# Performance work log

Hardware: AMD Instinct MI355X
Metric: run time of the kernel (lower is better)

## Reference

```python
import jax, jax.numpy as jnp
import numpy as np

IN_SIZE, R = 80, 5
D = 256  # hidden size used throughout
OUT = IN_SIZE * R  # 400


def gru_cell(x, h, Wih, Whh, bih, bhh):
    # torch.nn.GRUCell semantics
    gi = x @ Wih.T + bih
    gh = h @ Whh.T + bhh
    ir, iz, in_ = jnp.split(gi, 3, axis=-1)
    hr, hz, hn = jnp.split(gh, 3, axis=-1)
    r = jax.nn.sigmoid(ir + hr)
    z = jax.nn.sigmoid(iz + hz)
    n = jnp.tanh(in_ + r * hn)
    return (1.0 - z) * n + z * h


def setup_inputs() -> dict:
    key = jax.random.key(0)
    ks = jax.random.split(key, 32)
    s = 0.05
    inp = {
        'encoder_outputs': jax.random.normal(ks[0], (128, 512, D), jnp.float32),
        'inputs': jax.random.normal(ks[1], (128, 1000, IN_SIZE), jnp.float32),
        # Prenet: Linear(400,256), Linear(256,128)
        'W1': jax.random.normal(ks[2], (256, OUT)) * s, 'b1': jnp.zeros((256,)),
        'W2': jax.random.normal(ks[3], (128, 256)) * s, 'b2': jnp.zeros((128,)),
        # attn GRUCell(384 -> 256)
        'Wih_a': jax.random.normal(ks[4], (3 * D, 128 + D)) * s,
        'Whh_a': jax.random.normal(ks[5], (3 * D, D)) * s,
        'bih_a': jnp.zeros((3 * D,)), 'bhh_a': jnp.zeros((3 * D,)),
        # Bahdanau attention: query_layer (no bias) and v: Linear(256,1,no bias)
        'Wq': jax.random.normal(ks[6], (D, D)) * s,
        'v': jax.random.normal(ks[7], (D,)) * s,
        # memory_layer Linear(256,256,no bias)
        'Wm': jax.random.normal(ks[8], (D, D)) * s,
        # pre_rnn_dec_proj Linear(512,256)
        'Wp': jax.random.normal(ks[9], (D, 2 * D)) * s, 'bp': jnp.zeros((D,)),
        # two decoder GRUCells(256 -> 256)
        'Wih_d1': jax.random.normal(ks[10], (3 * D, D)) * s,
        'Whh_d1': jax.random.normal(ks[11], (3 * D, D)) * s,
        'bih_d1': jnp.zeros((3 * D,)), 'bhh_d1': jnp.zeros((3 * D,)),
        'Wih_d2': jax.random.normal(ks[12], (3 * D, D)) * s,
        'Whh_d2': jax.random.normal(ks[13], (3 * D, D)) * s,
        'bih_d2': jnp.zeros((3 * D,)), 'bhh_d2': jnp.zeros((3 * D,)),
        # mel projection Linear(256, 400)
        'Wmel': jax.random.normal(ks[14], (OUT, D)) * s, 'bmel': jnp.zeros((OUT,)),
    }
    return inp


def reference(encoder_outputs, inputs, W1, b1, W2, b2,
              Wih_a, Whh_a, bih_a, bhh_a, Wq, v, Wm, Wp, bp,
              Wih_d1, Whh_d1, bih_d1, bhh_d1,
              Wih_d2, Whh_d2, bih_d2, bhh_d2, Wmel, bmel):
    B = encoder_outputs.shape[0]
    processed_mem = encoder_outputs @ Wm.T               # (B, T_enc, D)
    # teacher forcing: (B, T_mel, in_size) -> (T_dec, B, in_size*r)
    x = inputs.reshape(B, inputs.shape[1] // R, -1).transpose(1, 0, 2)
    # decoder input at step t is frame t-1 (zeros at t=0)
    x_shift = jnp.concatenate([jnp.zeros_like(x[:1]), x[:-1]], axis=0)

    def step(carry, x_t):
        attn_h, h1, h2, ctx = carry
        # prenet (dropout disabled: eval-mode reference)
        pre = jax.nn.relu(x_t @ W1.T + b1)
        pre = jax.nn.relu(pre @ W2.T + b2)                # (B, 128)
        cell_in = jnp.concatenate([pre, ctx], axis=-1)    # (B, 384)
        attn_h = gru_cell(cell_in, attn_h, Wih_a, Whh_a, bih_a, bhh_a)
        q = attn_h @ Wq.T                                 # (B, D)
        logits = jnp.tanh(q[:, None, :] + processed_mem) @ v  # (B, T_enc)
        align = jax.nn.softmax(logits, axis=-1)
        ctx = jnp.einsum('bt,btd->bd', align, encoder_outputs)
        dec_in = jnp.concatenate([attn_h, ctx], axis=-1) @ Wp.T + bp
        h1 = gru_cell(dec_in, h1, Wih_d1, Whh_d1, bih_d1, bhh_d1)
        dec_in = h1 + dec_in
        h2 = gru_cell(dec_in, h2, Wih_d2, Whh_d2, bih_d2, bhh_d2)
        dec_in = h2 + dec_in
        out = dec_in @ Wmel.T + bmel                      # (B, 400)
        return (attn_h, h1, h2, ctx), (out, align)

    z = jnp.zeros((B, D), encoder_outputs.dtype)
    init = (z, z, z, z)
    _, (outs, aligns) = jax.lax.scan(step, init, x_shift)
    outputs = outs.transpose(1, 0, 2)       # (B, T_dec, 400)
    alignments = aligns.transpose(1, 0, 2)  # (B, T_dec, T_enc)
    return outputs, alignments
```

## Files before the change

kernel.cpp:

```cpp
#include <hip/hip_runtime.h>

typedef _Float16 h2f __attribute__((ext_vector_type(2)));

#define LOG2E 1.44269504088896f

__device__ __forceinline__ float fexp2(float x){ return __builtin_amdgcn_exp2f(x); }
__device__ __forceinline__ float frcp (float x){ return __builtin_amdgcn_rcpf(x); }
__device__ __forceinline__ float sigm (float x){ return frcp(1.f + fexp2(-LOG2E*x)); }
__device__ __forceinline__ float tanhf2(float x){
  x = fminf(15.f, fmaxf(-15.f, x));
  float e = fexp2(2.f*LOG2E*x);
  return (e-1.f)*frcp(e+1.f);
}
__device__ __forceinline__ unsigned pkh2(float a, float b){
  h2f h; h.x = (_Float16)a; h.y = (_Float16)b;
  return __builtin_bit_cast(unsigned, h);
}

#if __has_builtin(__builtin_amdgcn_fdot2)
__device__ __forceinline__ float dot2(unsigned a, unsigned b, float c){
  return __builtin_amdgcn_fdot2(__builtin_bit_cast(h2f,a), __builtin_bit_cast(h2f,b), c, false);
}
#else
__device__ __forceinline__ float dot2(unsigned a, unsigned b, float c){
  h2f ha=__builtin_bit_cast(h2f,a), hb=__builtin_bit_cast(h2f,b);
  return c + (float)ha.x*(float)hb.x + (float)ha.y*(float)hb.y;
}
#endif

__device__ __forceinline__ void dot8_2(uint4 w, uint4 x, float& a0, float& a1){
  a0 = dot2(w.x, x.x, a0); a1 = dot2(w.y, x.y, a1);
  a0 = dot2(w.z, x.z, a0); a1 = dot2(w.w, x.w, a1);
}

template<int N, int K8>
__device__ __forceinline__ float mv(const uint4* __restrict__ W, const uint4* __restrict__ xs, int n){
  float a0 = 0.f, a1 = 0.f;
  #pragma unroll 4
  for (int k8 = 0; k8 < K8; ++k8)
    dot8_2(W[k8*N + n], xs[k8], a0, a1);
  return a0 + a1;
}

template<int N, int K8, int C>
__device__ __forceinline__ float mvc(const uint4* __restrict__ W, const uint4* __restrict__ xs, int n){
  float a0 = 0.f, a1 = 0.f;
  int k8 = 0;
  #pragma unroll 1
  for (; k8 + C <= K8; k8 += C){
    uint4 w[C];
    #pragma unroll
    for (int i = 0; i < C; ++i) w[i] = W[(size_t)(k8+i)*N + n];
    #pragma unroll
    for (int i = 0; i < C; ++i) dot8_2(w[i], xs[k8+i], a0, a1);
  }
  if constexpr (K8 % C){
    constexpr int R = K8 % C;
    uint4 w[R];
    #pragma unroll
    for (int i = 0; i < R; ++i) w[i] = W[(size_t)(k8+i)*N + n];
    #pragma unroll
    for (int i = 0; i < R; ++i) dot8_2(w[i], xs[k8+i], a0, a1);
  }
  return a0 + a1;
}

static constexpr size_t OFF_W1   = 0;
static constexpr size_t OFF_W2   = 204800;
static constexpr size_t OFF_WIHA = 270336;
static constexpr size_t OFF_WHHA = 860160;
static constexpr size_t OFF_WQ   = 1253376;
static constexpr size_t OFF_WP   = 1384448;
static constexpr size_t OFF_WD1I = 1646592;
static constexpr size_t OFF_WD1H = 2039808;
static constexpr size_t OFF_WD2I = 2433024;
static constexpr size_t OFF_WD2H = 2826240;
static constexpr size_t OFF_WMEL = 3219456;
static constexpr size_t OFF_WM   = 3424256;
static constexpr size_t OFF_TPM  = 3555328;
static constexpr size_t OFF_ENCH = 37109760;

__global__ void pack_w(const float* __restrict__ src, uint4* __restrict__ dst, int N, int K8){
  int idx = blockIdx.x*blockDim.x + threadIdx.x;
  if (idx >= N*K8) return;
  int n = idx % N, k8 = idx / N;
  const float* s = src + (size_t)n*(K8*8) + k8*8;
  dst[idx] = make_uint4(pkh2(s[0],s[1]), pkh2(s[2],s[3]), pkh2(s[4],s[5]), pkh2(s[6],s[7]));
}

__global__ void conv_enc(const float* __restrict__ enc, unsigned* __restrict__ encH){
  size_t i = blockIdx.x*(size_t)blockDim.x + threadIdx.x;
  if (i >= (size_t)128*512*128) return;
  const float2 f = *(const float2*)(enc + 2*i);
  encH[i] = pkh2(f.x, f.y);
}

__global__ __launch_bounds__(1024) void pm_kernel(const float* __restrict__ enc,
    const uint4* __restrict__ Wmp, unsigned* __restrict__ tpm)
{
  int b = blockIdx.y, tc = blockIdx.x;
  int tid = threadIdx.x;
  __shared__ __align__(16) unsigned s_e[4][128];
  if (tid < 512){
    int r = tid >> 7, d2 = tid & 127;
    const float2 f = *(const float2*)(enc + ((size_t)b*512 + tc*4 + r)*256 + 2*d2);
    s_e[r][d2] = pkh2(f.x, f.y);
  }
  __syncthreads();
  int d = tid & 255, r = tid >> 8;
  float acc = mv<256,32>(Wmp, (const uint4*)s_e[r], d);
  float tq = tanhf2(acc);
  float hi = __shfl_down(tq, 1);
  if ((d & 1) == 0)
    tpm[(size_t)b*65536 + (size_t)(d>>1)*512 + (tc*4 + r)] = pkh2(tq, hi);
}

__global__ __launch_bounds__(1024) void decoder(
   const float* __restrict__ inputs,
   const float* __restrict__ b1, const float* __restrict__ b2,
   const float* __restrict__ biha, const float* __restrict__ bhha,
   const float* __restrict__ vvec, const float* __restrict__ bp,
   const float* __restrict__ bd1i, const float* __restrict__ bd1h,
   const float* __restrict__ bd2i, const float* __restrict__ bd2h,
   const float* __restrict__ bmel,
   const uint4* __restrict__ W1p, const uint4* __restrict__ W2p,
   const uint4* __restrict__ Wihap, const uint4* __restrict__ Whhap,
   const uint4* __restrict__ Wqp, const uint4* __restrict__ Wpp,
   const uint4* __restrict__ Wd1ip, const uint4* __restrict__ Wd1hp,
   const uint4* __restrict__ Wd2ip, const uint4* __restrict__ Wd2hp,
   const uint4* __restrict__ Wmelp,
   const unsigned* __restrict__ tpm, const unsigned* __restrict__ encH,
   float* __restrict__ out)
{
  const int tid = threadIdx.x;
  const int b = blockIdx.x;

  __shared__ __align__(16) unsigned s_x2[200];
  __shared__ __align__(16) unsigned s_p1[128];
  __shared__ __align__(16) unsigned s_cin2[192];
  __shared__ __align__(16) unsigned s_cat2[256];
  __shared__ __align__(16) unsigned s_di2[128];
  __shared__ __align__(16) unsigned s_h12[128];
  __shared__ __align__(16) unsigned s_h22[128];
  __shared__ float  s_gha[768], s_gh1[768], s_gh2[768];
  __shared__ float  s_g[768];
  __shared__ float  s_ahf[256];
  __shared__ float  s_h1f[256], s_h2f[256];
  __shared__ float  s_dif[256];
  __shared__ float4 s_tv[128];
  __shared__ float  s_lp[2][512];
  __shared__ float2 s_cp[8][128];
  __shared__ float  s_mvp[4][256];
  __shared__ float  s_align[512];
  __shared__ float  s_red[32];

  if (tid < 200) s_x2[tid] = 0u;
  if (tid < 192) s_cin2[tid] = 0u;
  if (tid < 256){ s_cat2[tid]=0u; s_ahf[tid]=0.f; s_h1f[tid]=0.f; s_h2f[tid]=0.f; }
  if (tid < 128){ s_h12[tid]=0u; s_h22[tid]=0u;
                  s_tv[tid].z = vvec[2*tid]; s_tv[tid].w = vvec[2*tid+1]; }
  __syncthreads();

  const unsigned* tpmB = tpm  + (size_t)b*65536;
  const unsigned* encB = encH + (size_t)b*65536;
  const float*    inB  = inputs + (size_t)b*80000;
  float* outMel = out + (size_t)b*200*400;
  float* outAl  = out + (size_t)10240000 + (size_t)b*200*512;

  for (int t = 0; t < 200; ++t){
    if (tid < 768){
      s_gha[tid] = mvc<768,32,8>(Whhap, (const uint4*)s_cat2, tid) + bhha[tid];
    } else {
      int n = tid - 768;
      float a = fmaxf(mvc<256,50,8>(W1p, (const uint4*)s_x2, n) + b1[n], 0.f);
      float aN = __shfl_down(a, 1);
      if (!(n&1)) s_p1[n>>1] = pkh2(a, aN);
    }
    __syncthreads();
    if (tid < 768){
      s_gh1[tid] = mvc<768,32,8>(Wd1hp, (const uint4*)s_h12, tid) + bd1h[tid];
    } else if (tid < 896){
      int n = tid - 768;
      float a = fmaxf(mvc<128,32,8>(W2p, (const uint4*)s_p1, n) + b2[n], 0.f);
      float aN = __shfl_down(a, 1);
      if (!(n&1)) s_cin2[n>>1] = pkh2(a, aN);
    }
    __syncthreads();
    if (tid < 768){
      float gi = mvc<768,48,8>(Wihap, (const uint4*)s_cin2, tid) + biha[tid];
      s_g[tid] = (tid < 512) ? sigm(gi + s_gha[tid]) : gi;
    }
    __syncthreads();
    if (tid < 256){
      float rr = s_g[tid], z = s_g[256+tid];
      float nv = tanhf2(s_g[512+tid] + rr*s_gha[512+tid]);
      float h  = nv + z*(s_ahf[tid] - nv);
      s_ahf[tid] = h;
      float hN = __shfl_down(h, 1);
      if (!(tid&1)) s_cat2[tid>>1] = pkh2(h, hN);
    }
    __syncthreads();
    if (tid < 256){
      float q = mvc<256,32,8>(Wqp, (const uint4*)s_cat2, tid);
      ((float*)&s_tv[tid>>1])[tid&1] = tanhf2(q);
    } else {
      int r = tid - 256;
      s_gh2[r] = mvc<768,32,8>(Wd2hp, (const uint4*)s_h22, r) + bd2h[r];
    }
    __syncthreads();
    {
      int tt = tid & 511, dh = tid >> 9;
      const unsigned* tp = tpmB + tt + (size_t)dh*64*512;
      float acc = 0.f;
      #pragma unroll 1
      for (int c = 0; c < 64; c += 16){
        unsigned tw[16];
        #pragma unroll
        for (int i = 0; i < 16; ++i) tw[i] = __builtin_nontemporal_load(&tp[(size_t)(c+i)*512]);
        #pragma unroll
        for (int i = 0; i < 16; ++i){
          h2f ta = __builtin_bit_cast(h2f, tw[i]);
          float4 tv = s_tv[dh*64 + c + i];
          float ta0 = (float)ta.x, ta1 = (float)ta.y;
          acc += tv.z*(ta0+tv.x)*frcp(1.f+ta0*tv.x)
               + tv.w*(ta1+tv.y)*frcp(1.f+ta1*tv.y);
        }
      }
      s_lp[dh][tt] = acc;
    }
    __syncthreads();
    {
      float lg = (tid < 512) ? (s_lp[0][tid] + s_lp[1][tid]) : -1e30f;
      float m = lg;
      #pragma unroll
      for (int off = 32; off >= 1; off >>= 1) m = fmaxf(m, __shfl_xor(m, off));
      if ((tid & 63) == 0) s_red[tid>>6] = m;
      __syncthreads();
      float M = fmaxf(fmaxf(fmaxf(s_red[0],s_red[1]),fmaxf(s_red[2],s_red[3])),
                      fmaxf(fmaxf(s_red[4],s_red[5]),fmaxf(s_red[6],s_red[7])));
      float e = (tid < 512) ? fexp2(LOG2E*(lg - M)) : 0.f;
      float s = e;
      #pragma unroll
      for (int off = 32; off >= 1; off >>= 1) s += __shfl_xor(s, off);
      if ((tid & 63) == 0) s_red[16+(tid>>6)] = s;
      __syncthreads();
      float S = (s_red[16]+s_red[17])+(s_red[18]+s_red[19])
              + (s_red[20]+s_red[21])+(s_red[22]+s_red[23]);
      float a = e * frcp(S);
      if (tid < 512){ s_align[tid] = a; __builtin_nontemporal_store(a, &outAl[(size_t)t*512 + tid]); }
    }
    __syncthreads();
    {
      int d2 = tid & 127, tc = tid >> 7;
      const unsigned* eb = encB + d2 + (size_t)tc*64*128;
      float ax = 0.f, ay = 0.f;
      #pragma unroll 1
      for (int c = 0; c < 64; c += 16){
        unsigned ew[16];
        #pragma unroll
        for (int i = 0; i < 16; ++i) ew[i] = __builtin_nontemporal_load(&eb[(size_t)(c+i)*128]);
        #pragma unroll
        for (int i = 0; i < 16; ++i){
          float a = s_align[tc*64 + c + i];
          h2f e2 = __builtin_bit_cast(h2f, ew[i]);
          ax += a*(float)e2.x; ay += a*(float)e2.y;
        }
      }
      s_cp[tc][d2] = make_float2(ax, ay);
    }
    __syncthreads();
    if (tid < 256){
      const float* cp = (const float*)s_cp;
      float c = 0.f;
      #pragma unroll
      for (int k = 0; k < 8; ++k) c += cp[k*256 + tid];
      float cN = __shfl_down(c, 1);
      if (!(tid&1)){ unsigned pk = pkh2(c, cN); s_cin2[64+(tid>>1)] = pk; s_cat2[128+(tid>>1)] = pk; }
    }
    __syncthreads();
    {
      int n = tid & 255, p = tid >> 8;
      const uint4* xs = (const uint4*)s_cat2;
      float a0 = 0.f, a1 = 0.f;
      #pragma unroll 1
      for (int c = 0; c < 16; c += 8){
        uint4 w[8];
        #pragma unroll
        for (int i = 0; i < 8; ++i) w[i] = Wpp[(size_t)(16*p+c+i)*256 + n];
        #pragma unroll
        for (int i = 0; i < 8; ++i) dot8_2(w[i], xs[16*p+c+i], a0, a1);
      }
      s_mvp[p][n] = a0 + a1;
    }
    __syncthreads();
    if (tid < 256){
      float di = s_mvp[0][tid]+s_mvp[1][tid]+s_mvp[2][tid]+s_mvp[3][tid] + bp[tid];
      s_dif[tid] = di;
      float dN = __shfl_down(di, 1);
      if (!(tid&1)) s_di2[tid>>1] = pkh2(di, dN);
    }
    __syncthreads();
    if (tid < 768){
      float gi = mvc<768,32,8>(Wd1ip, (const uint4*)s_di2, tid) + bd1i[tid];
      s_g[tid] = (tid < 512) ? sigm(gi + s_gh1[tid]) : gi;
    }
    __syncthreads();
    if (tid < 256){
      float rr = s_g[tid], z = s_g[256+tid];
      float nv = tanhf2(s_g[512+tid] + rr*s_gh1[512+tid]);
      float h  = nv + z*(s_h1f[tid] - nv);
      s_h1f[tid] = h;
      float di = s_dif[tid] + h; s_dif[tid] = di;
      float hN = __shfl_down(h, 1), dN = __shfl_down(di, 1);
      if (!(tid&1)){ s_h12[tid>>1] = pkh2(h, hN); s_di2[tid>>1] = pkh2(di, dN); }
    }
    __syncthreads();
    if (tid < 768){
      float gi = mvc<768,32,8>(Wd2ip, (const uint4*)s_di2, tid) + bd2i[tid];
      s_g[tid] = (tid < 512) ? sigm(gi + s_gh2[tid]) : gi;
    }
    __syncthreads();
    if (tid < 256){
      float rr = s_g[tid], z = s_g[256+tid];
      float nv = tanhf2(s_g[512+tid] + rr*s_gh2[512+tid]);
      float h  = nv + z*(s_h2f[tid] - nv);
      s_h2f[tid] = h;
      float di = s_dif[tid] + h; s_dif[tid] = di;
      float hN = __shfl_down(h, 1), dN = __shfl_down(di, 1);
      if (!(tid&1)){ s_h22[tid>>1] = pkh2(h, hN); s_di2[tid>>1] = pkh2(di, dN); }
    }
    __syncthreads();
    if (tid < 400){
      float a = mvc<400,32,8>(Wmelp, (const uint4*)s_di2, tid) + bmel[tid];
      __builtin_nontemporal_store(a, &outMel[(size_t)t*400 + tid]);
    } else if (tid >= 512 && tid < 712 && t+1 < 200){
      int j = tid - 512;
      const float2 f = *(const float2*)(inB + (size_t)t*400 + 2*j);
      s_x2[j] = pkh2(f.x, f.y);
    }
    __syncthreads();
  }
}

extern "C" void kernel_launch(void* const* d_in, const int* in_sizes, int n_in,
                              void* d_out, int out_size, void* d_ws, size_t ws_size,
                              hipStream_t stream){
  (void)in_sizes; (void)n_in; (void)out_size; (void)ws_size;
  const float* enc    = (const float*)d_in[0];
  const float* inputs = (const float*)d_in[1];
  const float* W1 = (const float*)d_in[2];   const float* b1 = (const float*)d_in[3];
  const float* W2 = (const float*)d_in[4];   const float* b2 = (const float*)d_in[5];
  const float* Wiha = (const float*)d_in[6]; const float* Whha = (const float*)d_in[7];
  const float* biha = (const float*)d_in[8]; const float* bhha = (const float*)d_in[9];
  const float* Wq = (const float*)d_in[10];  const float* v  = (const float*)d_in[11];
  const float* Wm = (const float*)d_in[12];
  const float* Wp = (const float*)d_in[13];  const float* bp = (const float*)d_in[14];
  const float* Wd1i = (const float*)d_in[15]; const float* Wd1h = (const float*)d_in[16];
  const float* bd1i = (const float*)d_in[17]; const float* bd1h = (const float*)d_in[18];
  const float* Wd2i = (const float*)d_in[19]; const float* Wd2h = (const float*)d_in[20];
  const float* bd2i = (const float*)d_in[21]; const float* bd2h = (const float*)d_in[22];
  const float* Wmel = (const float*)d_in[23]; const float* bmel = (const float*)d_in[24];

  char* ws = (char*)d_ws;
  uint4* W1p   = (uint4*)(ws + OFF_W1);
  uint4* W2p   = (uint4*)(ws + OFF_W2);
  uint4* Wihap = (uint4*)(ws + OFF_WIHA);
  uint4* Whhap = (uint4*)(ws + OFF_WHHA);
  uint4* Wqp   = (uint4*)(ws + OFF_WQ);
  uint4* Wpp   = (uint4*)(ws + OFF_WP);
  uint4* Wd1ip = (uint4*)(ws + OFF_WD1I);
  uint4* Wd1hp = (uint4*)(ws + OFF_WD1H);
  uint4* Wd2ip = (uint4*)(ws + OFF_WD2I);
  uint4* Wd2hp = (uint4*)(ws + OFF_WD2H);
  uint4* Wmelp = (uint4*)(ws + OFF_WMEL);
  uint4* Wmp   = (uint4*)(ws + OFF_WM);
  unsigned* tpm  = (unsigned*)(ws + OFF_TPM);
  unsigned* encH = (unsigned*)(ws + OFF_ENCH);

  auto P = [&](const float* s, uint4* dst, int N, int K){
    int k8 = K/8, tot = N*k8;
    pack_w<<<(tot+255)/256, 256, 0, stream>>>(s, dst, N, k8);
  };
  P(W1, W1p, 256, 400);   P(W2, W2p, 128, 256);
  P(Wiha, Wihap, 768, 384); P(Whha, Whhap, 768, 256);
  P(Wq, Wqp, 256, 256);   P(Wm, Wmp, 256, 256);
  P(Wp, Wpp, 256, 512);
  P(Wd1i, Wd1ip, 768, 256); P(Wd1h, Wd1hp, 768, 256);
  P(Wd2i, Wd2ip, 768, 256); P(Wd2h, Wd2hp, 768, 256);
  P(Wmel, Wmelp, 400, 256);

  conv_enc<<<32768, 256, 0, stream>>>(enc, encH);
  pm_kernel<<<dim3(128,128), 1024, 0, stream>>>(enc, Wmp, tpm);

  decoder<<<128, 1024, 0, stream>>>(inputs,
      b1, b2, biha, bhha, v, bp, bd1i, bd1h, bd2i, bd2h, bmel,
      W1p, W2p, Wihap, Whhap, Wqp, Wpp, Wd1ip, Wd1hp, Wd2ip, Wd2hp, Wmelp,
      tpm, encH, (float*)d_out);
}
```

Measured before the change: 9.522 ms.

## Software-pipeline weight loads and rebalance GRU matvec work across barrier phases

```diff
diff --git a/kernel.cpp b/kernel.cpp
--- a/kernel.cpp
+++ b/kernel.cpp
@@ -43,24 +43,27 @@
 }
 
 template<int N, int K8, int C>
-__device__ __forceinline__ float mvc(const uint4* __restrict__ W, const uint4* __restrict__ xs, int n){
+__device__ __forceinline__ float mvp(const uint4* __restrict__ W, const uint4* __restrict__ xs, int n){
+  static_assert(K8 % (2*C) == 0, "K8 must be divisible by 2C");
+  constexpr int NP = K8 / (2*C);
+  const uint4* Wn = W + n;
+  uint4 wa[C], wb[C];
+  #pragma unroll
+  for (int i = 0; i < C; ++i) wa[i] = Wn[(size_t)i*N];
   float a0 = 0.f, a1 = 0.f;
-  int k8 = 0;
   #pragma unroll 1
-  for (; k8 + C <= K8; k8 += C){
-    uint4 w[C];
+  for (int p = 0; p < NP; ++p){
+    const int k0 = p*2*C;
     #pragma unroll
-    for (int i = 0; i < C; ++i) w[i] = W[(size_t)(k8+i)*N + n];
+    for (int i = 0; i < C; ++i) wb[i] = Wn[(size_t)(k0 + C + i)*N];
     #pragma unroll
-    for (int i = 0; i < C; ++i) dot8_2(w[i], xs[k8+i], a0, a1);
-  }
-  if constexpr (K8 % C){
-    constexpr int R = K8 % C;
-    uint4 w[R];
+    for (int i = 0; i < C; ++i) dot8_2(wa[i], xs[k0 + i], a0, a1);
+    if (p + 1 < NP){
+      #pragma unroll
+      for (int i = 0; i < C; ++i) wa[i] = Wn[(size_t)(k0 + 2*C + i)*N];
+    }
     #pragma unroll
-    for (int i = 0; i < R; ++i) w[i] = W[(size_t)(k8+i)*N + n];
-    #pragma unroll
-    for (int i = 0; i < R; ++i) dot8_2(w[i], xs[k8+i], a0, a1);
+    for (int i = 0; i < C; ++i) dot8_2(wb[i], xs[k0 + C + i], a0, a1);
   }
   return a0 + a1;
 }
@@ -159,6 +162,7 @@
   if (tid < 256){ s_cat2[tid]=0u; s_ahf[tid]=0.f; s_h1f[tid]=0.f; s_h2f[tid]=0.f; }
   if (tid < 128){ s_h12[tid]=0u; s_h22[tid]=0u;
                   s_tv[tid].z = vvec[2*tid]; s_tv[tid].w = vvec[2*tid+1]; }
+  if (tid < 416) s_gha[tid] = bhha[tid];
   __syncthreads();
 
   const unsigned* tpmB = tpm  + (size_t)b*65536;
@@ -167,28 +171,41 @@
   float* outMel = out + (size_t)b*200*400;
   float* outAl  = out + (size_t)10240000 + (size_t)b*200*512;
 
+  unsigned pfA[16];
+
   for (int t = 0; t < 200; ++t){
-    if (tid < 768){
-      s_gha[tid] = mvc<768,32,8>(Whhap, (const uint4*)s_cat2, tid) + bhha[tid];
-    } else {
-      int n = tid - 768;
-      float a = fmaxf(mvc<256,50,8>(W1p, (const uint4*)s_x2, n) + b1[n], 0.f);
+    if (tid < 352){
+      int r = 416 + tid;
+      s_gha[r] = mvp<768,32,4>(Whhap, (const uint4*)s_cat2, r) + bhha[r];
+    } else if (tid < 608){
+      int n = tid - 352;
+      float a = fmaxf(mvp<256,50,5>(W1p, (const uint4*)s_x2, n) + b1[n], 0.f);
       float aN = __shfl_down(a, 1);
       if (!(n&1)) s_p1[n>>1] = pkh2(a, aN);
-    }
-    __syncthreads();
-    if (tid < 768){
-      s_gh1[tid] = mvc<768,32,8>(Wd1hp, (const uint4*)s_h12, tid) + bd1h[tid];
-    } else if (tid < 896){
-      int n = tid - 768;
-      float a = fmaxf(mvc<128,32,8>(W2p, (const uint4*)s_p1, n) + b2[n], 0.f);
+    } else {
+      int r = tid - 608;
+      s_gh1[r] = mvp<768,32,4>(Wd1hp, (const uint4*)s_h12, r) + bd1h[r];
+    }
+    __syncthreads();
+    if (tid < 352){
+      int r = 416 + tid;
+      s_gh1[r] = mvp<768,32,4>(Wd1hp, (const uint4*)s_h12, r) + bd1h[r];
+    } else if (tid < 480){
+      int n = tid - 352;
+      float a = fmaxf(mvp<128,32,4>(W2p, (const uint4*)s_p1, n) + b2[n], 0.f);
       float aN = __shfl_down(a, 1);
       if (!(n&1)) s_cin2[n>>1] = pkh2(a, aN);
+    } else if (tid < 992){
+      int r = tid - 480;
+      s_gh2[r] = mvp<768,32,4>(Wd2hp, (const uint4*)s_h22, r) + bd2h[r];
     }
     __syncthreads();
     if (tid < 768){
-      float gi = mvc<768,48,8>(Wihap, (const uint4*)s_cin2, tid) + biha[tid];
+      float gi = mvp<768,48,4>(Wihap, (const uint4*)s_cin2, tid) + biha[tid];
       s_g[tid] = (tid < 512) ? sigm(gi + s_gha[tid]) : gi;
+    } else {
+      int r = tid - 256;
+      s_gh2[r] = mvp<768,32,4>(Wd2hp, (const uint4*)s_h22, r) + bd2h[r];
     }
     __syncthreads();
     if (tid < 256){
@@ -200,36 +217,71 @@
       if (!(tid&1)) s_cat2[tid>>1] = pkh2(h, hN);
     }
     __syncthreads();
-    if (tid < 256){
-      float q = mvc<256,32,8>(Wqp, (const uint4*)s_cat2, tid);
+    {
+      const unsigned* tp = tpmB + (tid & 511) + (size_t)(tid >> 9)*32768;
+      #pragma unroll
+      for (int i = 0; i < 16; ++i) pfA[i] = __builtin_nontemporal_load(&tp[(size_t)i*512]);
+      int n = tid & 255, p = tid >> 8;
+      s_mvp[p][n] = mvp<256,8,4>(Wqp + (size_t)p*8*256, (const uint4*)s_cat2 + p*8, n);
+    }
+    __syncthreads();
+    if (tid < 256){
+      float q = s_mvp[0][tid]+s_mvp[1][tid]+s_mvp[2][tid]+s_mvp[3][tid];
       ((float*)&s_tv[tid>>1])[tid&1] = tanhf2(q);
-    } else {
-      int r = tid - 256;
-      s_gh2[r] = mvc<768,32,8>(Wd2hp, (const uint4*)s_h22, r) + bd2h[r];
     }
     __syncthreads();
     {
       int tt = tid & 511, dh = tid >> 9;
-      const unsigned* tp = tpmB + tt + (size_t)dh*64*512;
+      const unsigned* tp = tpmB + tt + (size_t)dh*32768;
+      unsigned pfB[16];
+      #pragma unroll
+      for (int i = 0; i < 16; ++i) pfB[i] = __builtin_nontemporal_load(&tp[(size_t)(16+i)*512]);
       float acc = 0.f;
-      #pragma unroll 1
-      for (int c = 0; c < 64; c += 16){
-        unsigned tw[16];
-        #pragma unroll
-        for (int i = 0; i < 16; ++i) tw[i] = __builtin_nontemporal_load(&tp[(size_t)(c+i)*512]);
-        #pragma unroll
-        for (int i = 0; i < 16; ++i){
-          h2f ta = __builtin_bit_cast(h2f, tw[i]);
-          float4 tv = s_tv[dh*64 + c + i];
-          float ta0 = (float)ta.x, ta1 = (float)ta.y;
-          acc += tv.z*(ta0+tv.x)*frcp(1.f+ta0*tv.x)
-               + tv.w*(ta1+tv.y)*frcp(1.f+ta1*tv.y);
-        }
+      #pragma unroll
+      for (int i = 0; i < 16; ++i){
+        h2f ta = __builtin_bit_cast(h2f, pfA[i]);
+        float4 tv = s_tv[dh*64 + i];
+        float ta0 = (float)ta.x, ta1 = (float)ta.y;
+        acc += tv.z*(ta0+tv.x)*frcp(1.f+ta0*tv.x)
+             + tv.w*(ta1+tv.y)*frcp(1.f+ta1*tv.y);
+      }
+      #pragma unroll
+      for (int i = 0; i < 16; ++i) pfA[i] = __builtin_nontemporal_load(&tp[(size_t)(32+i)*512]);
+      #pragma unroll
+      for (int i = 0; i < 16; ++i){
+        h2f ta = __builtin_bit_cast(h2f, pfB[i]);
+        float4 tv = s_tv[dh*64 + 16 + i];
+        float ta0 = (float)ta.x, ta1 = (float)ta.y;
+        acc += tv.z*(ta0+tv.x)*frcp(1.f+ta0*tv.x)
+             + tv.w*(ta1+tv.y)*frcp(1.f+ta1*tv.y);
+      }
+      #pragma unroll
+      for (int i = 0; i < 16; ++i) pfB[i] = __builtin_nontemporal_load(&tp[(size_t)(48+i)*512]);
+      #pragma unroll
+      for (int i = 0; i < 16; ++i){
+        h2f ta = __builtin_bit_cast(h2f, pfA[i]);
+        float4 tv = s_tv[dh*64 + 32 + i];
+        float ta0 = (float)ta.x, ta1 = (float)ta.y;
+        acc += tv.z*(ta0+tv.x)*frcp(1.f+ta0*tv.x)
+             + tv.w*(ta1+tv.y)*frcp(1.f+ta1*tv.y);
+      }
+      #pragma unroll
+      for (int i = 0; i < 16; ++i){
+        h2f ta = __builtin_bit_cast(h2f, pfB[i]);
+        float4 tv = s_tv[dh*64 + 48 + i];
+        float ta0 = (float)ta.x, ta1 = (float)ta.y;
+        acc += tv.z*(ta0+tv.x)*frcp(1.f+ta0*tv.x)
+             + tv.w*(ta1+tv.y)*frcp(1.f+ta1*tv.y);
       }
       s_lp[dh][tt] = acc;
     }
     __syncthreads();
+    unsigned pfE[16];
     {
+      const unsigned* eb = encB + (tid & 127) + (size_t)(tid >> 7)*8192;
+      #pragma unroll
+      for (int i = 0; i < 16; ++i) pfE[i] = __builtin_nontemporal_load(&eb[(size_t)i*128]);
+
       float lg = (tid < 512) ? (s_lp[0][tid] + s_lp[1][tid]) : -1e30f;
       float m = lg;
       #pragma unroll
@@ -252,19 +304,38 @@
     __syncthreads();
     {
       int d2 = tid & 127, tc = tid >> 7;
-      const unsigned* eb = encB + d2 + (size_t)tc*64*128;
+      const unsigned* eb = encB + d2 + (size_t)tc*8192;
+      unsigned pfF[16];
+      #pragma unroll
+      for (int i = 0; i < 16; ++i) pfF[i] = __builtin_nontemporal_load(&eb[(size_t)(16+i)*128]);
       float ax = 0.f, ay = 0.f;
-      #pragma unroll 1
-      for (int c = 0; c < 64; c += 16){
-        unsigned ew[16];
-        #pragma unroll
-        for (int i = 0; i < 16; ++i) ew[i] = __builtin_nontemporal_load(&eb[(size_t)(c+i)*128]);
-        #pragma unroll
-        for (int i = 0; i < 16; ++i){
-          float a = s_align[tc*64 + c + i];
-          h2f e2 = __builtin_bit_cast(h2f, ew[i]);
-          ax += a*(float)e2.x; ay += a*(float)e2.y;
-        }
+      #pragma unroll
+      for (int i = 0; i < 16; ++i){
+        float a = s_align[tc*64 + i];
+        h2f e2 = __builtin_bit_cast(h2f, pfE[i]);
+        ax += a*(float)e2.x; ay += a*(float)e2.y;
+      }
+      #pragma unroll
+      for (int i = 0; i < 16; ++i) pfE[i] = __builtin_nontemporal_load(&eb[(size_t)(32+i)*128]);
+      #pragma unroll
+      for (int i = 0; i < 16; ++i){
+        float a = s_align[tc*64 + 16 + i];
+        h2f e2 = __builtin_bit_cast(h2f, pfF[i]);
+        ax += a*(float)e2.x; ay += a*(float)e2.y;
+      }
+      #pragma unroll
+      for (int i = 0; i < 16; ++i) pfF[i] = __builtin_nontemporal_load(&eb[(size_t)(48+i)*128]);
+      #pragma unroll
+      for (int i = 0; i < 16; ++i){
+        float a = s_align[tc*64 + 32 + i];
+        h2f e2 = __builtin_bit_cast(h2f, pfE[i]);
+        ax += a*(float)e2.x; ay += a*(float)e2.y;
+      }
+      #pragma unroll
+      for (int i = 0; i < 16; ++i){
+        float a = s_align[tc*64 + 48 + i];
+        h2f e2 = __builtin_bit_cast(h2f, pfF[i]);
+        ax += a*(float)e2.x; ay += a*(float)e2.y;
       }
       s_cp[tc][d2] = make_float2(ax, ay);
     }
@@ -280,17 +351,7 @@
     __syncthreads();
     {
       int n = tid & 255, p = tid >> 8;
-      const uint4* xs = (const uint4*)s_cat2;
-      float a0 = 0.f, a1 = 0.f;
-      #pragma unroll 1
-      for (int c = 0; c < 16; c += 8){
-        uint4 w[8];
-        #pragma unroll
-        for (int i = 0; i < 8; ++i) w[i] = Wpp[(size_t)(16*p+c+i)*256 + n];
-        #pragma unroll
-        for (int i = 0; i < 8; ++i) dot8_2(w[i], xs[16*p+c+i], a0, a1);
-      }
-      s_mvp[p][n] = a0 + a1;
+      s_mvp[p][n] = mvp<256,16,4>(Wpp + (size_t)p*16*256, (const uint4*)s_cat2 + p*16, n);
     }
     __syncthreads();
     if (tid < 256){
@@ -301,7 +362,7 @@
     }
     __syncthreads();
     if (tid < 768){
-      float gi = mvc<768,32,8>(Wd1ip, (const uint4*)s_di2, tid) + bd1i[tid];
+      float gi = mvp<768,32,4>(Wd1ip, (const uint4*)s_di2, tid) + bd1i[tid];
       s_g[tid] = (tid < 512) ? sigm(gi + s_gh1[tid]) : gi;
     }
     __syncthreads();
@@ -316,7 +377,7 @@
     }
     __syncthreads();
     if (tid < 768){
-      float gi = mvc<768,32,8>(Wd2ip, (const uint4*)s_di2, tid) + bd2i[tid];
+      float gi = mvp<768,32,4>(Wd2ip, (const uint4*)s_di2, tid) + bd2i[tid];
       s_g[tid] = (tid < 512) ? sigm(gi + s_gh2[tid]) : gi;
     }
     __syncthreads();
@@ -331,12 +392,19 @@
     }
     __syncthreads();
     if (tid < 400){
-      float a = mvc<400,32,8>(Wmelp, (const uint4*)s_di2, tid) + bmel[tid];
+      float a = mvp<400,32,4>(Wmelp, (const uint4*)s_di2, tid) + bmel[tid];
       __builtin_nontemporal_store(a, &outMel[(size_t)t*400 + tid]);
-    } else if (tid >= 512 && tid < 712 && t+1 < 200){
-      int j = tid - 512;
-      const float2 f = *(const float2*)(inB + (size_t)t*400 + 2*j);
-      s_x2[j] = pkh2(f.x, f.y);
+    } else if (tid >= 400 && tid < 600){
+      if (t < 199){
+        int j = tid - 400;
+        const float2 f = *(const float2*)(inB + (size_t)t*400 + 2*j);
+        s_x2[j] = pkh2(f.x, f.y);
+      }
+    } else if (tid >= 608){
+      if (t < 199){
+        int r = tid - 608;
+        s_gha[r] = mvp<768,32,4>(Whhap, (const uint4*)s_cat2, r) + bhha[r];
+      }
     }
     __syncthreads();
   }
```

Measured after the change: 25.50 ms. +167.8%, slower.

## Hoist prenet and mel projection out of recurrent decoder into parallel kernels

Applied to the files above, without the earlier changes.

```diff
diff --git a/kernel.cpp b/kernel.cpp
--- a/kernel.cpp
+++ b/kernel.cpp
@@ -115,28 +115,72 @@
     tpm[(size_t)b*65536 + (size_t)(d>>1)*512 + (tc*4 + r)] = pkh2(tq, hi);
 }
 
-__global__ __launch_bounds__(1024) void decoder(
-   const float* __restrict__ inputs,
-   const float* __restrict__ b1, const float* __restrict__ b2,
+__global__ __launch_bounds__(256) void prenet_kernel(
+    const float* __restrict__ inputs,
+    const float* __restrict__ b1, const float* __restrict__ b2,
+    const uint4* __restrict__ W1p, const uint4* __restrict__ W2p,
+    float* __restrict__ out)
+{
+  int t = blockIdx.x, b = blockIdx.y;
+  int tid = threadIdx.x;
+  __shared__ __align__(16) unsigned s_x[200];
+  __shared__ __align__(16) unsigned s_p1[128];
+  __shared__ float s_a[256];
+  if (tid < 200){
+    unsigned xv = 0u;
+    if (t > 0){
+      const float2 f = *(const float2*)(inputs + (size_t)b*80000 + (size_t)(t-1)*400 + 2*tid);
+      xv = pkh2(f.x, f.y);
+    }
+    s_x[tid] = xv;
+  }
+  __syncthreads();
+  float a = fmaxf(mv<256,50>(W1p, (const uint4*)s_x, tid) + b1[tid], 0.f);
+  s_a[tid] = a;
+  __syncthreads();
+  if (tid < 128) s_p1[tid] = pkh2(s_a[2*tid], s_a[2*tid+1]);
+  __syncthreads();
+  if (tid < 128){
+    float p = fmaxf(mv<128,32>(W2p, (const uint4*)s_p1, tid) + b2[tid], 0.f);
+    float pN = __shfl_down(p, 1);
+    if (!(tid & 1)){
+      unsigned* dst = (unsigned*)(out + (size_t)10240000 + ((size_t)b*200 + t)*512);
+      dst[tid>>1] = pkh2(p, pN);
+    }
+  }
+}
+
+__global__ __launch_bounds__(512) void mel_kernel(
+    const float* __restrict__ bmel, const uint4* __restrict__ Wmelp,
+    float* __restrict__ out)
+{
+  int t = blockIdx.x, b = blockIdx.y;
+  int tid = threadIdx.x;
+  __shared__ __align__(16) unsigned s_d[128];
+  float* po = out + ((size_t)b*200 + t)*400;
+  if (tid < 128) s_d[tid] = ((const unsigned*)po)[tid];
+  __syncthreads();
+  if (tid < 400){
+    float r = mvc<400,32,8>(Wmelp, (const uint4*)s_d, tid) + bmel[tid];
+    __builtin_nontemporal_store(r, &po[tid]);
+  }
+}
+
+__global__ __launch_bounds__(1024, 1) void decoder(
    const float* __restrict__ biha, const float* __restrict__ bhha,
    const float* __restrict__ vvec, const float* __restrict__ bp,
    const float* __restrict__ bd1i, const float* __restrict__ bd1h,
    const float* __restrict__ bd2i, const float* __restrict__ bd2h,
-   const float* __restrict__ bmel,
-   const uint4* __restrict__ W1p, const uint4* __restrict__ W2p,
    const uint4* __restrict__ Wihap, const uint4* __restrict__ Whhap,
    const uint4* __restrict__ Wqp, const uint4* __restrict__ Wpp,
    const uint4* __restrict__ Wd1ip, const uint4* __restrict__ Wd1hp,
    const uint4* __restrict__ Wd2ip, const uint4* __restrict__ Wd2hp,
-   const uint4* __restrict__ Wmelp,
    const unsigned* __restrict__ tpm, const unsigned* __restrict__ encH,
    float* __restrict__ out)
 {
   const int tid = threadIdx.x;
   const int b = blockIdx.x;
 
-  __shared__ __align__(16) unsigned s_x2[200];
-  __shared__ __align__(16) unsigned s_p1[128];
   __shared__ __align__(16) unsigned s_cin2[192];
   __shared__ __align__(16) unsigned s_cat2[256];
   __shared__ __align__(16) unsigned s_di2[128];
@@ -144,17 +188,15 @@
   __shared__ __align__(16) unsigned s_h22[128];
   __shared__ float  s_gha[768], s_gh1[768], s_gh2[768];
   __shared__ float  s_g[768];
-  __shared__ float  s_ahf[256];
-  __shared__ float  s_h1f[256], s_h2f[256];
+  __shared__ float  s_ahf[256], s_h1f[256], s_h2f[256];
   __shared__ float  s_dif[256];
   __shared__ float4 s_tv[128];
   __shared__ float  s_lp[2][512];
   __shared__ float2 s_cp[8][128];
   __shared__ float  s_mvp[4][256];
   __shared__ float  s_align[512];
-  __shared__ float  s_red[32];
-
-  if (tid < 200) s_x2[tid] = 0u;
+  __shared__ float  s_red[16];
+
   if (tid < 192) s_cin2[tid] = 0u;
   if (tid < 256){ s_cat2[tid]=0u; s_ahf[tid]=0.f; s_h1f[tid]=0.f; s_h2f[tid]=0.f; }
   if (tid < 128){ s_h12[tid]=0u; s_h22[tid]=0u;
@@ -163,32 +205,32 @@
 
   const unsigned* tpmB = tpm  + (size_t)b*65536;
   const unsigned* encB = encH + (size_t)b*65536;
-  const float*    inB  = inputs + (size_t)b*80000;
   float* outMel = out + (size_t)b*200*400;
   float* outAl  = out + (size_t)10240000 + (size_t)b*200*512;
 
   for (int t = 0; t < 200; ++t){
     if (tid < 768){
       s_gha[tid] = mvc<768,32,8>(Whhap, (const uint4*)s_cat2, tid) + bhha[tid];
+    } else if (tid < 960){
+      int r = tid - 768;
+      s_gh2[r] = mvc<768,32,8>(Wd2hp, (const uint4*)s_h22, r) + bd2h[r];
     } else {
-      int n = tid - 768;
-      float a = fmaxf(mvc<256,50,8>(W1p, (const uint4*)s_x2, n) + b1[n], 0.f);
-      float aN = __shfl_down(a, 1);
-      if (!(n&1)) s_p1[n>>1] = pkh2(a, aN);
+      s_cin2[tid-960] = ((const unsigned*)(outAl + (size_t)t*512))[tid-960];
     }
     __syncthreads();
     if (tid < 768){
       s_gh1[tid] = mvc<768,32,8>(Wd1hp, (const uint4*)s_h12, tid) + bd1h[tid];
-    } else if (tid < 896){
-      int n = tid - 768;
-      float a = fmaxf(mvc<128,32,8>(W2p, (const uint4*)s_p1, n) + b2[n], 0.f);
-      float aN = __shfl_down(a, 1);
-      if (!(n&1)) s_cin2[n>>1] = pkh2(a, aN);
+    } else {
+      int r = 192 + tid - 768;
+      s_gh2[r] = mvc<768,32,8>(Wd2hp, (const uint4*)s_h22, r) + bd2h[r];
     }
     __syncthreads();
     if (tid < 768){
       float gi = mvc<768,48,8>(Wihap, (const uint4*)s_cin2, tid) + biha[tid];
       s_g[tid] = (tid < 512) ? sigm(gi + s_gha[tid]) : gi;
+    } else {
+      int r = 448 + tid - 768;
+      s_gh2[r] = mvc<768,32,8>(Wd2hp, (const uint4*)s_h22, r) + bd2h[r];
     }
     __syncthreads();
     if (tid < 256){
@@ -198,19 +240,24 @@
       s_ahf[tid] = h;
       float hN = __shfl_down(h, 1);
       if (!(tid&1)) s_cat2[tid>>1] = pkh2(h, hN);
-    }
-    __syncthreads();
-    if (tid < 256){
-      float q = mvc<256,32,8>(Wqp, (const uint4*)s_cat2, tid);
+    } else if (tid < 320){
+      int r = 704 + tid - 256;
+      s_gh2[r] = mvc<768,32,8>(Wd2hp, (const uint4*)s_h22, r) + bd2h[r];
+    }
+    __syncthreads();
+    if (tid < 512){
+      int n = tid & 255, p = tid >> 8;
+      s_mvp[p][n] = mvc<256,16,8>(Wqp + (size_t)p*16*256, (const uint4*)s_cat2 + p*16, n);
+    }
+    __syncthreads();
+    if (tid < 256){
+      float q = s_mvp[0][tid] + s_mvp[1][tid];
       ((float*)&s_tv[tid>>1])[tid&1] = tanhf2(q);
-    } else {
-      int r = tid - 256;
-      s_gh2[r] = mvc<768,32,8>(Wd2hp, (const uint4*)s_h22, r) + bd2h[r];
     }
     __syncthreads();
     {
       int tt = tid & 511, dh = tid >> 9;
-      const unsigned* tp = tpmB + tt + (size_t)dh*64*512;
+      const unsigned* tp = tpmB + tt + (size_t)dh*32768;
       float acc = 0.f;
       #pragma unroll 1
       for (int c = 0; c < 64; c += 16){
@@ -229,30 +276,27 @@
       s_lp[dh][tt] = acc;
     }
     __syncthreads();
-    {
-      float lg = (tid < 512) ? (s_lp[0][tid] + s_lp[1][tid]) : -1e30f;
-      float m = lg;
-      #pragma unroll
-      for (int off = 32; off >= 1; off >>= 1) m = fmaxf(m, __shfl_xor(m, off));
-      if ((tid & 63) == 0) s_red[tid>>6] = m;
-      __syncthreads();
-      float M = fmaxf(fmaxf(fmaxf(s_red[0],s_red[1]),fmaxf(s_red[2],s_red[3])),
-                      fmaxf(fmaxf(s_red[4],s_red[5]),fmaxf(s_red[6],s_red[7])));
-      float e = (tid < 512) ? fexp2(LOG2E*(lg - M)) : 0.f;
-      float s = e;
+    float ee = 0.f;
+    if (tid < 512){
+      float lg = s_lp[0][tid] + s_lp[1][tid];
+      ee = fexp2(LOG2E*lg);
+      float s = ee;
       #pragma unroll
       for (int off = 32; off >= 1; off >>= 1) s += __shfl_xor(s, off);
-      if ((tid & 63) == 0) s_red[16+(tid>>6)] = s;
-      __syncthreads();
-      float S = (s_red[16]+s_red[17])+(s_red[18]+s_red[19])
-              + (s_red[20]+s_red[21])+(s_red[22]+s_red[23]);
-      float a = e * frcp(S);
-      if (tid < 512){ s_align[tid] = a; __builtin_nontemporal_store(a, &outAl[(size_t)t*512 + tid]); }
+      if ((tid & 63) == 0) s_red[tid>>6] = s;
+    }
+    __syncthreads();
+    if (tid < 512){
+      float S = (s_red[0]+s_red[1])+(s_red[2]+s_red[3])
+              + (s_red[4]+s_red[5])+(s_red[6]+s_red[7]);
+      float a = ee * frcp(S);
+      s_align[tid] = a;
+      __builtin_nontemporal_store(a, &outAl[(size_t)t*512 + tid]);
     }
     __syncthreads();
     {
       int d2 = tid & 127, tc = tid >> 7;
-      const unsigned* eb = encB + d2 + (size_t)tc*64*128;
+      const unsigned* eb = encB + d2 + (size_t)tc*8192;
       float ax = 0.f, ay = 0.f;
       #pragma unroll 1
       for (int c = 0; c < 64; c += 16){
@@ -280,17 +324,7 @@
     __syncthreads();
     {
       int n = tid & 255, p = tid >> 8;
-      const uint4* xs = (const uint4*)s_cat2;
-      float a0 = 0.f, a1 = 0.f;
-      #pragma unroll 1
-      for (int c = 0; c < 16; c += 8){
-        uint4 w[8];
-        #pragma unroll
-        for (int i = 0; i < 8; ++i) w[i] = Wpp[(size_t)(16*p+c+i)*256 + n];
-        #pragma unroll
-        for (int i = 0; i < 8; ++i) dot8_2(w[i], xs[16*p+c+i], a0, a1);
-      }
-      s_mvp[p][n] = a0 + a1;
+      s_mvp[p][n] = mvc<256,16,8>(Wpp + (size_t)p*16*256, (const uint4*)s_cat2 + p*16, n);
     }
     __syncthreads();
     if (tid < 256){
@@ -325,18 +359,14 @@
       float nv = tanhf2(s_g[512+tid] + rr*s_gh2[512+tid]);
       float h  = nv + z*(s_h2f[tid] - nv);
       s_h2f[tid] = h;
-      float di = s_dif[tid] + h; s_dif[tid] = di;
+      float di = s_dif[tid] + h;
       float hN = __shfl_down(h, 1), dN = __shfl_down(di, 1);
-      if (!(tid&1)){ s_h22[tid>>1] = pkh2(h, hN); s_di2[tid>>1] = pkh2(di, dN); }
-    }
-    __syncthreads();
-    if (tid < 400){
-      float a = mvc<400,32,8>(Wmelp, (const uint4*)s_di2, tid) + bmel[tid];
-      __builtin_nontemporal_store(a, &outMel[(size_t)t*400 + tid]);
-    } else if (tid >= 512 && tid < 712 && t+1 < 200){
-      int j = tid - 512;
-      const float2 f = *(const float2*)(inB + (size_t)t*400 + 2*j);
-      s_x2[j] = pkh2(f.x, f.y);
+      if (!(tid&1)){
+        unsigned dpk = pkh2(di, dN);
+        s_h22[tid>>1] = pkh2(h, hN);
+        s_di2[tid>>1] = dpk;
+        ((unsigned*)(outMel + (size_t)t*400))[tid>>1] = dpk;
+      }
     }
     __syncthreads();
   }
@@ -391,9 +421,12 @@
 
   conv_enc<<<32768, 256, 0, stream>>>(enc, encH);
   pm_kernel<<<dim3(128,128), 1024, 0, stream>>>(enc, Wmp, tpm);
-
-  decoder<<<128, 1024, 0, stream>>>(inputs,
-      b1, b2, biha, bhha, v, bp, bd1i, bd1h, bd2i, bd2h, bmel,
-      W1p, W2p, Wihap, Whhap, Wqp, Wpp, Wd1ip, Wd1hp, Wd2ip, Wd2hp, Wmelp,
+  prenet_kernel<<<dim3(200,128), 256, 0, stream>>>(inputs, b1, b2, W1p, W2p, (float*)d_out);
+
+  decoder<<<128, 1024, 0, stream>>>(
+      biha, bhha, v, bp, bd1i, bd1h, bd2i, bd2h,
+      Wihap, Whhap, Wqp, Wpp, Wd1ip, Wd1hp, Wd2ip, Wd2hp,
       tpm, encH, (float*)d_out);
-}
+
+  mel_kernel<<<dim3(200,128), 512, 0, stream>>>(bmel, Wmelp, (float*)d_out);
+}
```

New measurement: 8.842 ms (median of 5 runs). -7.1%, faster.
